# Performance work log

Hardware: AMD Instinct MI355X
Metric: run time of the kernel (lower is better)

Reference implementation:

```python
import jax, jax.numpy as jnp
import numpy as np

B, T, C, H = 2, 2048, 1024, 16
HID = 4096
EPS = 1e-5
NEG_INF = float('-inf')


def layer_norm(x, w, b):
    mu = jnp.mean(x, axis=-1, keepdims=True)
    var = jnp.mean((x - mu) ** 2, axis=-1, keepdims=True)
    return (x - mu) / jnp.sqrt(var + EPS) * w + b


def setup_inputs() -> dict:
    key = jax.random.key(0)
    ks = jax.random.split(key, 12)
    s = lambda fan_in: 1.0 / np.sqrt(fan_in)
    return {
        'x': jax.random.normal(ks[0], (B, T, C), dtype=jnp.float32),
        'mask': jax.random.randint(ks[1], (B, T), 0, 2) > 0,
        'attn_w': jax.random.normal(ks[2], (C, 3 * C), dtype=jnp.float32) * s(C),
        'attn_b': jnp.zeros((3 * C,), dtype=jnp.float32),
        'proj_w': jax.random.normal(ks[3], (C, C), dtype=jnp.float32) * s(C),
        'proj_b': jnp.zeros((C,), dtype=jnp.float32),
        'ln1_w': jnp.ones((C,), dtype=jnp.float32),
        'ln1_b': jnp.zeros((C,), dtype=jnp.float32),
        'lin1_w': jax.random.normal(ks[4], (C, HID), dtype=jnp.float32) * s(C),
        'lin1_b': jnp.zeros((HID,), dtype=jnp.float32),
        'lin2_w': jax.random.normal(ks[5], (HID, C), dtype=jnp.float32) * s(HID),
        'lin2_b': jnp.zeros((C,), dtype=jnp.float32),
        'ln2_w': jnp.ones((C,), dtype=jnp.float32),
        'ln2_b': jnp.zeros((C,), dtype=jnp.float32),
    }


def reference(x, mask, attn_w, attn_b, proj_w, proj_b, ln1_w, ln1_b,
              lin1_w, lin1_b, lin2_w, lin2_b, ln2_w, ln2_b):
    D = C // H
    # fused QKV projection
    qkv = x @ attn_w + attn_b                      # [B,T,3C]
    q, k, v = jnp.split(qkv, 3, axis=-1)
    q = q.reshape(B, T, H, D).transpose(0, 2, 1, 3)  # [B,H,T,D]
    k = k.reshape(B, T, H, D).transpose(0, 2, 1, 3)
    v = v.reshape(B, T, H, D).transpose(0, 2, 1, 3)
    scale = 1.0 / jnp.sqrt(jnp.asarray(D, dtype=q.dtype))
    scores = jnp.einsum('bhqd,bhkd->bhqk', q, k) * scale  # [B,H,T,T]
    # bidirectional padding mask with forced-true first key column
    m2d = mask[:, None, :] & mask[:, :, None]       # [B,T,T]
    m2d = m2d.at[:, :, 0].set(True)
    bias = jnp.where(m2d, 0.0, NEG_INF).astype(scores.dtype)
    scores = scores + bias[:, None, :, :]
    w = jax.nn.softmax(scores, axis=-1)
    w = jnp.nan_to_num(w, nan=0.0, posinf=0.0, neginf=0.0)
    y = jnp.einsum('bhqk,bhkd->bhqd', w, v)
    y = y.transpose(0, 2, 1, 3).reshape(B, T, C)
    y = y @ proj_w + proj_b
    # residual + post-LN, then MLP + residual + post-LN
    h = layer_norm(x + y, ln1_w, ln1_b)
    ff = jax.nn.gelu(h @ lin1_w + lin1_b, approximate=False) @ lin2_w + lin2_b
    return layer_norm(h + ff, ln2_w, ln2_b)
```

## Files before the change

### kernel.cpp

```cpp
#include <hip/hip_runtime.h>
#include <hip/hip_bf16.h>
#include <math.h>

typedef __attribute__((ext_vector_type(4))) float f32x4;
typedef __attribute__((ext_vector_type(8))) __bf16 bf16x8v;
typedef __attribute__((ext_vector_type(4))) __bf16 bf16x4v;
typedef __attribute__((ext_vector_type(4))) short s16x4;
typedef __attribute__((ext_vector_type(4))) unsigned short u16x4;

#define AS1(p) ((const __attribute__((address_space(1))) void*)(p))
#define AS3(p) ((__attribute__((address_space(3))) void*)(p))

__device__ __forceinline__ unsigned short f2bf(float f) {
  union { __bf16 b; unsigned short u; } cv;
  cv.b = (__bf16)f;
  return cv.u;
}

__device__ __forceinline__ f32x4 mfma32(bf16x8v a, bf16x8v b, f32x4 c) {
  return __builtin_amdgcn_mfma_f32_16x16x32_bf16(a, b, c, 0, 0, 0);
}

__device__ __forceinline__ f32x4 mfma16(s16x4 a, s16x4 b, f32x4 c) {
#if __has_builtin(__builtin_amdgcn_mfma_f32_16x16x16bf16_1k)
  return __builtin_amdgcn_mfma_f32_16x16x16bf16_1k(a, b, c, 0, 0, 0);
#elif __has_builtin(__builtin_amdgcn_mfma_f32_16x16x16_bf16)
  bf16x4v av, bv;
  __builtin_memcpy(&av, &a, 8);
  __builtin_memcpy(&bv, &b, 8);
  return __builtin_amdgcn_mfma_f32_16x16x16_bf16(av, bv, c, 0, 0, 0);
#else
  asm volatile("v_mfma_f32_16x16x16_bf16 %0, %1, %2, %0\n\ts_nop 7\n\ts_nop 7\n\ts_nop 7"
               : "+v"(c) : "v"(a), "v"(b));
  return c;
#endif
}

__device__ __forceinline__ void async_copy16(const void* g, void* l) {
  __builtin_amdgcn_global_load_lds(AS1(g), AS3(l), 16, 0, 0);
}

__global__ __launch_bounds__(256) void cvt_bf16_kernel(const float* __restrict__ in,
                                                       unsigned short* __restrict__ out, int n4) {
  int i = blockIdx.x * 256 + threadIdx.x;
  if (i < n4) {
    f32x4 v = ((const f32x4*)in)[i];
    u16x4 o;
    o.x = f2bf(v.x); o.y = f2bf(v.y); o.z = f2bf(v.z); o.w = f2bf(v.w);
    ((u16x4*)out)[i] = o;
  }
}

__global__ __launch_bounds__(256) void wtrans_kernel(const float* __restrict__ W,
                                                     unsigned short* __restrict__ Wt,
                                                     int Kd, int Nd) {
  __shared__ float t[32][33];
  int tx = threadIdx.x & 31, ty = threadIdx.x >> 5;
  int bx = blockIdx.x, by = blockIdx.y;
  for (int i = 0; i < 4; ++i) {
    int r = by * 32 + ty + i * 8, c = bx * 32 + tx;
    t[ty + i * 8][tx] = W[(size_t)r * Nd + c];
  }
  __syncthreads();
  for (int i = 0; i < 4; ++i) {
    int nn = bx * 32 + ty + i * 8, kk = by * 32 + tx;
    Wt[(size_t)nn * Kd + kk] = f2bf(t[tx][ty + i * 8]);
  }
}

template <int EPI>
__global__ __launch_bounds__(512, 2) void gemm256(const unsigned short* __restrict__ A,
                                                  const unsigned short* __restrict__ Bt,
                                                  const float* __restrict__ bias,
                                                  unsigned short* __restrict__ out,
                                                  int M, int N, int Kd, int gx) {
  __shared__ __align__(16) unsigned short Al[2][256 * 64];
  __shared__ __align__(16) unsigned short Bl[2][256 * 64];
  int tid = threadIdx.x, wid = tid >> 6, lane = tid & 63;
  int lo = lane & 15, hi = lane >> 4;
  int wm = wid >> 2, wn = wid & 3;

  int wg = blockIdx.x, nwg = gridDim.x;
  int cpx = nwg >> 3;
  int swz = (wg & 7) * cpx + (wg >> 3);
  int m0 = (swz / gx) * 256, n0 = (swz % gx) * 256;

  f32x4 acc[8][4];
#pragma unroll
  for (int mf = 0; mf < 8; ++mf)
#pragma unroll
    for (int nf = 0; nf < 4; ++nf) acc[mf][nf] = f32x4{0.f, 0.f, 0.f, 0.f};

  int nkt = Kd >> 6;

  auto stageAB = [&](int buf, int kt) {
#pragma unroll
    for (int i = 0; i < 4; ++i) {
      int G = (wid * 4 + i) * 64 + lane;
      int row = G >> 3, c16 = G & 7;
      int csw = ((c16 ^ (row & 7)) << 3);
      const unsigned short* ga = A + ((size_t)(m0 + row)) * Kd + kt * 64 + csw;
      async_copy16(ga, &Al[buf][(wid * 4 + i) * 512]);
      const unsigned short* gb = Bt + ((size_t)(n0 + row)) * Kd + kt * 64 + csw;
      async_copy16(gb, &Bl[buf][(wid * 4 + i) * 512]);
    }
  };

  stageAB(0, 0);
  int cur = 0;
  for (int t = 0; t < nkt; ++t) {
    __builtin_amdgcn_s_barrier();
    int nx = t + 1 < nkt ? t + 1 : nkt - 1;
    stageAB(cur ^ 1, nx);
    asm volatile("s_waitcnt vmcnt(8)" ::: "memory");
    __builtin_amdgcn_sched_barrier(0);

    bf16x8v bfr[4][2];
#pragma unroll
    for (int nf = 0; nf < 4; ++nf) {
      int rb = wn * 64 + nf * 16 + lo;
#pragma unroll
      for (int kh = 0; kh < 2; ++kh)
        bfr[nf][kh] = *(const bf16x8v*)&Bl[cur][rb * 64 + (((kh * 4 + hi) ^ (rb & 7)) << 3)];
    }
#pragma unroll
    for (int q = 0; q < 4; ++q) {
      bf16x8v afr[2][2];
#pragma unroll
      for (int m2 = 0; m2 < 2; ++m2) {
        int ra = wm * 128 + (q * 2 + m2) * 16 + lo;
#pragma unroll
        for (int kh = 0; kh < 2; ++kh)
          afr[m2][kh] = *(const bf16x8v*)&Al[cur][ra * 64 + (((kh * 4 + hi) ^ (ra & 7)) << 3)];
      }
      __builtin_amdgcn_s_setprio(1);
#pragma unroll
      for (int m2 = 0; m2 < 2; ++m2)
#pragma unroll
        for (int nf = 0; nf < 4; ++nf) {
          acc[q * 2 + m2][nf] = mfma32(afr[m2][0], bfr[nf][0], acc[q * 2 + m2][nf]);
          acc[q * 2 + m2][nf] = mfma32(afr[m2][1], bfr[nf][1], acc[q * 2 + m2][nf]);
        }
      __builtin_amdgcn_s_setprio(0);
    }
    cur ^= 1;
  }

#pragma unroll
  for (int nf = 0; nf < 4; ++nf) {
    int col = n0 + wn * 64 + nf * 16 + lo;
    float bv = bias[col];
#pragma unroll
    for (int mf = 0; mf < 8; ++mf) {
      int row0 = m0 + wm * 128 + mf * 16 + hi * 4;
#pragma unroll
      for (int j = 0; j < 4; ++j) {
        float v = acc[mf][nf][j] + bv;
        if (EPI == 2) v = 0.5f * v * (1.f + erff(v * 0.70710678118654752f));
        out[(size_t)(row0 + j) * N + col] = f2bf(v);
      }
    }
  }
}

template <int EPI>
__global__ __launch_bounds__(256) void gemm_bt(const unsigned short* __restrict__ A,
                                               const unsigned short* __restrict__ Bt,
                                               const float* __restrict__ bias,
                                               void* __restrict__ out,
                                               int M, int N, int Kd, int gx) {
  __shared__ __align__(16) unsigned short As[3][128 * 32];
  __shared__ __align__(16) unsigned short Bs[3][128 * 32];
  int tid = threadIdx.x, wid = tid >> 6, lane = tid & 63;
  int lo = lane & 15, hi = lane >> 4;

  int wg = blockIdx.x, nwg = gridDim.x;
  int cpx = nwg >> 3;
  int swz = (wg & 7) * cpx + (wg >> 3);
  int m0 = (swz / gx) * 128, n0 = (swz % gx) * 128;

  int wm = wid >> 1, wn = wid & 1;
  f32x4 acc[4][4];
  for (int m = 0; m < 4; ++m)
    for (int n = 0; n < 4; ++n) acc[m][n] = f32x4{0.f, 0.f, 0.f, 0.f};
  int sr = lane >> 2;
  int sc = (lane & 3) * 8;
  int nkt = Kd >> 5;

  auto stage = [&](int buf, int kt) {
    int k0 = kt * 32;
#pragma unroll
    for (int i = 0; i < 2; ++i) {
      int ch = wid * 2 + i;
      const unsigned short* ga = A + ((size_t)(m0 + ch * 16 + sr)) * Kd + k0 + sc;
      async_copy16(ga, &As[buf][ch * 512]);
      const unsigned short* gb = Bt + ((size_t)(n0 + ch * 16 + sr)) * Kd + k0 + sc;
      async_copy16(gb, &Bs[buf][ch * 512]);
    }
  };

  stage(0, 0);
  stage(1, 1);
  stage(2, 2);
  int cur = 0;
  for (int kt = 0; kt < nkt; ++kt) {
    asm volatile("s_waitcnt vmcnt(8)" ::: "memory");
    asm volatile("s_barrier" ::: "memory");
    __builtin_amdgcn_sched_barrier(0);
    bf16x8v af[4], bf_[4];
#pragma unroll
    for (int m = 0; m < 4; ++m)
      af[m] = *(const bf16x8v*)&As[cur][(wm * 64 + m * 16 + lo) * 32 + hi * 8];
#pragma unroll
    for (int n = 0; n < 4; ++n)
      bf_[n] = *(const bf16x8v*)&Bs[cur][(wn * 64 + n * 16 + lo) * 32 + hi * 8];
#pragma unroll
    for (int m = 0; m < 4; ++m)
#pragma unroll
      for (int n = 0; n < 4; ++n)
        acc[m][n] = mfma32(af[m], bf_[n], acc[m][n]);
    __builtin_amdgcn_sched_barrier(0);
    asm volatile("s_barrier" ::: "memory");
    int nx = kt + 3;
    nx = nx < nkt ? nx : nkt - 1;
    stage(cur, nx);
    cur = cur + 1;
    cur = cur == 3 ? 0 : cur;
  }

#pragma unroll
  for (int n = 0; n < 4; ++n) {
    int col = n0 + wn * 64 + n * 16 + lo;
    float bv = bias ? bias[col] : 0.f;
#pragma unroll
    for (int m = 0; m < 4; ++m) {
      int row0 = m0 + wm * 64 + m * 16 + hi * 4;
#pragma unroll
      for (int j = 0; j < 4; ++j) {
        float v = acc[m][n][j] + bv;
        size_t idx = (size_t)(row0 + j) * N + col;
        if (EPI == 1) ((float*)out)[idx] = v;
        else          ((unsigned short*)out)[idx] = f2bf(v);
      }
    }
  }
}

__global__ __launch_bounds__(256) void reshape_qk_kernel(const unsigned short* __restrict__ qkv,
                                                         unsigned short* __restrict__ Q,
                                                         unsigned short* __restrict__ K) {
  int idx = blockIdx.x * 256 + threadIdx.x;
  int row = idx >> 9;
  int g = idx & 511;
  int col = g * 4;
  int sec = col >> 10;
  int cc = col & 1023;
  int h = cc >> 6, d = cc & 63;
  int b = row >> 11, t = row & 2047;
  u16x4 v = *(const u16x4*)&qkv[(size_t)row * 3072 + col];
  unsigned short* dst = sec ? K : Q;
  *(u16x4*)&dst[(((size_t)(b * 16 + h)) * 2048 + t) * 64 + d] = v;
}

__global__ __launch_bounds__(256) void vtrans_kernel(const unsigned short* __restrict__ qkv,
                                                     unsigned short* __restrict__ Vt) {
  __shared__ unsigned short t[32][33];
  int tx = threadIdx.x & 31, ty = threadIdx.x >> 5;
  int bx = blockIdx.x, dt = blockIdx.y, bh = blockIdx.z;
  int b = bh >> 4, h = bh & 15;
  for (int i = 0; i < 4; ++i) {
    int trow = bx * 32 + ty + i * 8;
    t[ty + i * 8][tx] = qkv[((size_t)(b * 2048 + trow)) * 3072 + 2048 + h * 64 + dt * 32 + tx];
  }
  __syncthreads();
  for (int i = 0; i < 4; ++i) {
    int d = dt * 32 + ty + i * 8;
    int trow = bx * 32 + tx;
    Vt[((size_t)bh * 64 + d) * 2048 + trow] = t[tx][ty + i * 8];
  }
}

__global__ __launch_bounds__(256) void attn_kernel(const unsigned short* __restrict__ Q,
                                                   const unsigned short* __restrict__ Kt,
                                                   const unsigned short* __restrict__ Vt,
                                                   const int* __restrict__ mask,
                                                   unsigned short* __restrict__ Y) {
  __shared__ __align__(16) unsigned short Kl[2][4096];
  __shared__ __align__(16) unsigned short Vl[2][4096];
  __shared__ float sbias[2048];

  int qt = blockIdx.x, bh = blockIdx.y;
  int b = bh >> 4, h = bh & 15;
  int tid = threadIdx.x, wv = tid >> 6, lane = tid & 63;
  int lo = lane & 15, hi = lane >> 4;

  for (int k = tid; k < 2048; k += 256) {
    int mk = mask[b * 2048 + k];
    sbias[k] = (mk != 0 || k == 0) ? 0.f : -1e30f;
  }

  int r8 = lane >> 3;
  int jsrc = (((lane & 7) ^ r8) << 4);
  const size_t kvbase = (size_t)bh * 2048;

  auto stage = [&](int buf, int kt2) {
    int kbase = kt2 * 64;
#pragma unroll
    for (int i = 0; i < 2; ++i) {
      int r = i * 32 + wv * 8 + r8;
      const unsigned short* gk = Kt + (kvbase + kbase + r) * 64 + (jsrc >> 1);
      async_copy16(gk, (char*)Kl + buf * 8192 + i * 4096 + wv * 1024);
      const unsigned short* gv = Vt + ((size_t)bh * 64 + r) * 2048 + kbase + (jsrc >> 1);
      async_copy16(gv, (char*)Vl + buf * 8192 + i * 4096 + wv * 1024);
    }
  };

  int qrow = qt * 64 + wv * 16 + lo;
  size_t qoff = (kvbase + qrow) * 64;
  bf16x8v Qf0 = *(const bf16x8v*)(Q + qoff + hi * 8);
  bf16x8v Qf1 = *(const bf16x8v*)(Q + qoff + 32 + hi * 8);
  float qm = (mask[b * 2048 + qrow] != 0) ? -16.f : -1e30f;

  const float scale2 = 0.125f * 1.44269504088896340736f;
  float l_run = 0.f;
  f32x4 acc[4];
#pragma unroll
  for (int c = 0; c < 4; ++c) acc[c] = f32x4{0.f, 0.f, 0.f, 0.f};

  stage(0, 0);
  stage(1, 1);
  asm volatile("s_waitcnt lgkmcnt(0)" ::: "memory");

  int sw = (lo & 7) << 4;
  int cur = 0;
  for (int kt = 0; kt < 32; ++kt) {
    asm volatile("s_waitcnt vmcnt(4)" ::: "memory");
    asm volatile("s_barrier" ::: "memory");
    __builtin_amdgcn_sched_barrier(0);
    int kbase = kt * 64;

    f32x4 s4[4];
#pragma unroll
    for (int kb = 0; kb < 4; ++kb) {
      const char* kr = (const char*)Kl + cur * 8192 + (kb * 16 + lo) * 128;
      bf16x8v K0 = *(const bf16x8v*)(kr + ((hi * 16) ^ sw));
      bf16x8v K1 = *(const bf16x8v*)(kr + ((64 + hi * 16) ^ sw));
      f32x4 z = f32x4{0.f, 0.f, 0.f, 0.f};
      z = mfma32(K0, Qf0, z);
      z = mfma32(K1, Qf1, z);
      s4[kb] = z;
    }

    float p[16];
#pragma unroll
    for (int kb = 0; kb < 4; ++kb) {
      f32x4 bb = *(const f32x4*)&sbias[kbase + kb * 16 + hi * 4];
#pragma unroll
      for (int r = 0; r < 4; ++r)
        p[kb * 4 + r] = fmaf(s4[kb][r], scale2, bb[r] + qm);
    }
    if (kt == 0)
      p[0] = (hi == 0) ? fmaf(s4[0][0], scale2, -16.f) : p[0];
#pragma unroll
    for (int i = 0; i < 16; ++i) p[i] = exp2f(p[i]);
    float ls0 = 0.f, ls1 = 0.f;
#pragma unroll
    for (int i = 0; i < 8; ++i) { ls0 += p[i]; ls1 += p[8 + i]; }
    l_run += ls0 + ls1;

    union { __bf16 b[4]; s16x4 s4v; } pk[4];
#pragma unroll
    for (int kb = 0; kb < 4; ++kb)
#pragma unroll
      for (int r = 0; r < 4; ++r) pk[kb].b[r] = (__bf16)p[kb * 4 + r];

#pragma unroll
    for (int c = 0; c < 4; ++c) {
      const char* vr = (const char*)Vl + cur * 8192 + (c * 16 + lo) * 128;
#pragma unroll
      for (int kk = 0; kk < 4; ++kk) {
        s16x4 V0 = *(const s16x4*)(vr + ((kk * 32 + hi * 8) ^ sw));
        acc[c] = mfma16(V0, pk[kk].s4v, acc[c]);
      }
    }
    __builtin_amdgcn_sched_barrier(0);
    asm volatile("s_barrier" ::: "memory");
    int nx = kt + 2;
    nx = nx < 32 ? nx : 31;
    stage(cur, nx);
    cur ^= 1;
  }

  l_run += __shfl_xor(l_run, 16);
  l_run += __shfl_xor(l_run, 32);
  float invl = 1.f / l_run;
  size_t yrow = ((size_t)(b * 2048 + qrow)) * 1024 + h * 64;
#pragma unroll
  for (int c = 0; c < 4; ++c)
#pragma unroll
    for (int r = 0; r < 4; ++r)
      Y[yrow + c * 16 + hi * 4 + r] = f2bf(acc[c][r] * invl);
}

__global__ __launch_bounds__(256) void ln_kernel(const float* __restrict__ A,
                                                 const float* __restrict__ Bsrc,
                                                 const float* __restrict__ w,
                                                 const float* __restrict__ bias,
                                                 float* __restrict__ outF,
                                                 unsigned short* __restrict__ outB) {
  int row = blockIdx.x, tid = threadIdx.x;
  f32x4 r = ((const f32x4*)A)[row * 256 + tid] + ((const f32x4*)Bsrc)[row * 256 + tid];
  float s = r.x + r.y + r.z + r.w;
  float q = r.x * r.x + r.y * r.y + r.z * r.z + r.w * r.w;
  for (int off = 1; off < 64; off <<= 1) {
    s += __shfl_xor(s, off);
    q += __shfl_xor(q, off);
  }
  __shared__ float ls[4], lq[4];
  int wid = tid >> 6, lane = tid & 63;
  if (lane == 0) { ls[wid] = s; lq[wid] = q; }
  __syncthreads();
  s = ls[0] + ls[1] + ls[2] + ls[3];
  q = lq[0] + lq[1] + lq[2] + lq[3];
  float mu = s * (1.f / 1024.f);
  float var = q * (1.f / 1024.f) - mu * mu;
  float rstd = rsqrtf(var + 1e-5f);
  f32x4 wv = ((const f32x4*)w)[tid];
  f32x4 bv = ((const f32x4*)bias)[tid];
  f32x4 o = (r - mu) * rstd * wv + bv;
  if (outF) ((f32x4*)outF)[row * 256 + tid] = o;
  if (outB) {
    u16x4 ob;
    ob.x = f2bf(o.x); ob.y = f2bf(o.y); ob.z = f2bf(o.z); ob.w = f2bf(o.w);
    ((u16x4*)outB)[row * 256 + tid] = ob;
  }
}

extern "C" void kernel_launch(void* const* d_in, const int* in_sizes, int n_in,
                              void* d_out, int out_size, void* d_ws, size_t ws_size,
                              hipStream_t stream) {
  const float* x      = (const float*)d_in[0];
  const int*   mask   = (const int*)d_in[1];
  const float* attn_w = (const float*)d_in[2];
  const float* attn_b = (const float*)d_in[3];
  const float* proj_w = (const float*)d_in[4];
  const float* proj_b = (const float*)d_in[5];
  const float* ln1_w  = (const float*)d_in[6];
  const float* ln1_b  = (const float*)d_in[7];
  const float* lin1_w = (const float*)d_in[8];
  const float* lin1_b = (const float*)d_in[9];
  const float* lin2_w = (const float*)d_in[10];
  const float* lin2_b = (const float*)d_in[11];
  const float* ln2_w  = (const float*)d_in[12];
  const float* ln2_b  = (const float*)d_in[13];
  float* out = (float*)d_out;

  char* ws = (char*)d_ws;
  size_t off = 0;
  auto alloc = [&](size_t bytes) { char* p = ws + off; off += (bytes + 255) & ~(size_t)255; return p; };

  unsigned short* attn_wT = (unsigned short*)alloc((size_t)3072 * 1024 * 2);
  unsigned short* proj_wT = (unsigned short*)alloc((size_t)1024 * 1024 * 2);
  unsigned short* lin1_wT = (unsigned short*)alloc((size_t)4096 * 1024 * 2);
  unsigned short* lin2_wT = (unsigned short*)alloc((size_t)1024 * 4096 * 2);
  char* regionA = alloc((size_t)3 * 8388608);
  char* regionB = alloc((size_t)8388608);
  char* regionC = alloc((size_t)25165824);
  float* h_f32  = (float*)alloc((size_t)4096 * 1024 * 4);
  unsigned short* h_bf16 = (unsigned short*)alloc((size_t)4096 * 1024 * 2);
  float* mlp2   = (float*)alloc((size_t)4096 * 1024 * 4);

  unsigned short* Qb  = (unsigned short*)regionA;
  unsigned short* Kb  = (unsigned short*)(regionA + 8388608);
  unsigned short* Vtb = (unsigned short*)(regionA + 16777216);
  unsigned short* ff1 = (unsigned short*)regionA;
  unsigned short* xb  = (unsigned short*)regionB;
  unsigned short* qkv = (unsigned short*)regionC;
  unsigned short* Yb  = (unsigned short*)regionC;
  float* proj_out     = (float*)(regionC + 8388608);

  wtrans_kernel<<<dim3(96, 32), 256, 0, stream>>>(attn_w, attn_wT, 1024, 3072);
  wtrans_kernel<<<dim3(32, 32), 256, 0, stream>>>(proj_w, proj_wT, 1024, 1024);
  wtrans_kernel<<<dim3(128, 32), 256, 0, stream>>>(lin1_w, lin1_wT, 1024, 4096);
  wtrans_kernel<<<dim3(32, 128), 256, 0, stream>>>(lin2_w, lin2_wT, 4096, 1024);
  cvt_bf16_kernel<<<4096, 256, 0, stream>>>(x, xb, 4096 * 1024 / 4);

  gemm256<0><<<192, 512, 0, stream>>>(xb, attn_wT, attn_b, qkv, 4096, 3072, 1024, 12);
  reshape_qk_kernel<<<8192, 256, 0, stream>>>(qkv, Qb, Kb);
  vtrans_kernel<<<dim3(64, 2, 32), 256, 0, stream>>>(qkv, Vtb);

  attn_kernel<<<dim3(32, 32), 256, 0, stream>>>(Qb, Kb, Vtb, mask, Yb);

  gemm_bt<1><<<256, 256, 0, stream>>>(Yb, proj_wT, proj_b, proj_out, 4096, 1024, 1024, 8);
  ln_kernel<<<4096, 256, 0, stream>>>(x, proj_out, ln1_w, ln1_b, h_f32, h_bf16);

  gemm256<2><<<256, 512, 0, stream>>>(h_bf16, lin1_wT, lin1_b, ff1, 4096, 4096, 1024, 16);
  gemm_bt<1><<<256, 256, 0, stream>>>(ff1, lin2_wT, lin2_b, mlp2, 4096, 1024, 4096, 8);
  ln_kernel<<<4096, 256, 0, stream>>>(h_f32, mlp2, ln2_w, ln2_b, out, nullptr);
}
```

Baseline: 440.7 us.

## Read Q/K directly from qkv, split-K lin2 GEMM, widen attention blocks

The Q/K reshape kernel is removed, and attention now loads Q and K straight from the packed qkv buffer using 512-thread blocks that each cover 128 query rows. The lin2 GEMM is split along K into two halves that write separate fp32 partials, doubling the grid to 512 workgroups, and the second layernorm sums both partials. Scheduling barriers and setprio hints are also dropped from the GEMM and attention loops. The changes target a launch plus a memory pass and low occupancy in lin2, at the cost of an extra fp32 partial buffer and strided K loads.

```diff
diff --git a/kernel.cpp b/kernel.cpp
--- a/kernel.cpp
+++ b/kernel.cpp
@@ -113,7 +113,6 @@
     int nx = t + 1 < nkt ? t + 1 : nkt - 1;
     stageAB(cur ^ 1, nx);
     asm volatile("s_waitcnt vmcnt(8)" ::: "memory");
-    __builtin_amdgcn_sched_barrier(0);
 
     bf16x8v bfr[4][2];
 #pragma unroll
@@ -133,7 +132,6 @@
         for (int kh = 0; kh < 2; ++kh)
           afr[m2][kh] = *(const bf16x8v*)&Al[cur][ra * 64 + (((kh * 4 + hi) ^ (ra & 7)) << 3)];
       }
-      __builtin_amdgcn_s_setprio(1);
 #pragma unroll
       for (int m2 = 0; m2 < 2; ++m2)
 #pragma unroll
@@ -141,7 +139,6 @@
           acc[q * 2 + m2][nf] = mfma32(afr[m2][0], bfr[nf][0], acc[q * 2 + m2][nf]);
           acc[q * 2 + m2][nf] = mfma32(afr[m2][1], bfr[nf][1], acc[q * 2 + m2][nf]);
         }
-      __builtin_amdgcn_s_setprio(0);
     }
     cur ^= 1;
   }
@@ -163,21 +160,29 @@
   }
 }
 
-template <int EPI>
+template <int EPI, int SPLIT>
 __global__ __launch_bounds__(256) void gemm_bt(const unsigned short* __restrict__ A,
                                                const unsigned short* __restrict__ Bt,
                                                const float* __restrict__ bias,
-                                               void* __restrict__ out,
-                                               int M, int N, int Kd, int gx) {
+                                               void* __restrict__ out0,
+                                               void* __restrict__ out1,
+                                               int M, int N, int Kd, int ldk, int gx) {
   __shared__ __align__(16) unsigned short As[3][128 * 32];
   __shared__ __align__(16) unsigned short Bs[3][128 * 32];
   int tid = threadIdx.x, wid = tid >> 6, lane = tid & 63;
   int lo = lane & 15, hi = lane >> 4;
 
   int wg = blockIdx.x, nwg = gridDim.x;
+  int kp = 0;
+  if (SPLIT) { kp = wg & 1; wg >>= 1; nwg >>= 1; }
   int cpx = nwg >> 3;
   int swz = (wg & 7) * cpx + (wg >> 3);
   int m0 = (swz / gx) * 128, n0 = (swz % gx) * 128;
+
+  const unsigned short* Ab = A + (SPLIT ? kp * Kd : 0);
+  const unsigned short* Bb = Bt + (SPLIT ? kp * Kd : 0);
+  void* out = (SPLIT && kp) ? out1 : out0;
+  const float* bz = (SPLIT && kp) ? nullptr : bias;
 
   int wm = wid >> 1, wn = wid & 1;
   f32x4 acc[4][4];
@@ -192,9 +197,9 @@
 #pragma unroll
     for (int i = 0; i < 2; ++i) {
       int ch = wid * 2 + i;
-      const unsigned short* ga = A + ((size_t)(m0 + ch * 16 + sr)) * Kd + k0 + sc;
+      const unsigned short* ga = Ab + ((size_t)(m0 + ch * 16 + sr)) * ldk + k0 + sc;
       async_copy16(ga, &As[buf][ch * 512]);
-      const unsigned short* gb = Bt + ((size_t)(n0 + ch * 16 + sr)) * Kd + k0 + sc;
+      const unsigned short* gb = Bb + ((size_t)(n0 + ch * 16 + sr)) * ldk + k0 + sc;
       async_copy16(gb, &Bs[buf][ch * 512]);
     }
   };
@@ -206,7 +211,6 @@
   for (int kt = 0; kt < nkt; ++kt) {
     asm volatile("s_waitcnt vmcnt(8)" ::: "memory");
     asm volatile("s_barrier" ::: "memory");
-    __builtin_amdgcn_sched_barrier(0);
     bf16x8v af[4], bf_[4];
 #pragma unroll
     for (int m = 0; m < 4; ++m)
@@ -219,7 +223,6 @@
 #pragma unroll
       for (int n = 0; n < 4; ++n)
         acc[m][n] = mfma32(af[m], bf_[n], acc[m][n]);
-    __builtin_amdgcn_sched_barrier(0);
     asm volatile("s_barrier" ::: "memory");
     int nx = kt + 3;
     nx = nx < nkt ? nx : nkt - 1;
@@ -231,7 +234,7 @@
 #pragma unroll
   for (int n = 0; n < 4; ++n) {
     int col = n0 + wn * 64 + n * 16 + lo;
-    float bv = bias ? bias[col] : 0.f;
+    float bv = bz ? bz[col] : 0.f;
 #pragma unroll
     for (int m = 0; m < 4; ++m) {
       int row0 = m0 + wm * 64 + m * 16 + hi * 4;
@@ -244,22 +247,6 @@
       }
     }
   }
-}
-
-__global__ __launch_bounds__(256) void reshape_qk_kernel(const unsigned short* __restrict__ qkv,
-                                                         unsigned short* __restrict__ Q,
-                                                         unsigned short* __restrict__ K) {
-  int idx = blockIdx.x * 256 + threadIdx.x;
-  int row = idx >> 9;
-  int g = idx & 511;
-  int col = g * 4;
-  int sec = col >> 10;
-  int cc = col & 1023;
-  int h = cc >> 6, d = cc & 63;
-  int b = row >> 11, t = row & 2047;
-  u16x4 v = *(const u16x4*)&qkv[(size_t)row * 3072 + col];
-  unsigned short* dst = sec ? K : Q;
-  *(u16x4*)&dst[(((size_t)(b * 16 + h)) * 2048 + t) * 64 + d] = v;
 }
 
 __global__ __launch_bounds__(256) void vtrans_kernel(const unsigned short* __restrict__ qkv,
@@ -280,8 +267,7 @@
   }
 }
 
-__global__ __launch_bounds__(256) void attn_kernel(const unsigned short* __restrict__ Q,
-                                                   const unsigned short* __restrict__ Kt,
+__global__ __launch_bounds__(512) void attn_kernel(const unsigned short* __restrict__ qkv,
                                                    const unsigned short* __restrict__ Vt,
                                                    const int* __restrict__ mask,
                                                    unsigned short* __restrict__ Y) {
@@ -294,31 +280,28 @@
   int tid = threadIdx.x, wv = tid >> 6, lane = tid & 63;
   int lo = lane & 15, hi = lane >> 4;
 
-  for (int k = tid; k < 2048; k += 256) {
+  for (int k = tid; k < 2048; k += 512) {
     int mk = mask[b * 2048 + k];
     sbias[k] = (mk != 0 || k == 0) ? 0.f : -1e30f;
   }
 
-  int r8 = lane >> 3;
-  int jsrc = (((lane & 7) ^ r8) << 4);
-  const size_t kvbase = (size_t)bh * 2048;
+  int r = tid >> 3;
+  int slot = tid & 7;
+  int jb = ((slot ^ (r & 7)) << 4) >> 1;
 
   auto stage = [&](int buf, int kt2) {
     int kbase = kt2 * 64;
-#pragma unroll
-    for (int i = 0; i < 2; ++i) {
-      int r = i * 32 + wv * 8 + r8;
-      const unsigned short* gk = Kt + (kvbase + kbase + r) * 64 + (jsrc >> 1);
-      async_copy16(gk, (char*)Kl + buf * 8192 + i * 4096 + wv * 1024);
-      const unsigned short* gv = Vt + ((size_t)bh * 64 + r) * 2048 + kbase + (jsrc >> 1);
-      async_copy16(gv, (char*)Vl + buf * 8192 + i * 4096 + wv * 1024);
-    }
+    const unsigned short* gk =
+        qkv + ((size_t)(b * 2048 + kbase + r)) * 3072 + 1024 + h * 64 + jb;
+    async_copy16(gk, (char*)Kl + buf * 8192 + wv * 1024);
+    const unsigned short* gv = Vt + ((size_t)(bh * 64 + r)) * 2048 + kbase + jb;
+    async_copy16(gv, (char*)Vl + buf * 8192 + wv * 1024);
   };
 
-  int qrow = qt * 64 + wv * 16 + lo;
-  size_t qoff = (kvbase + qrow) * 64;
-  bf16x8v Qf0 = *(const bf16x8v*)(Q + qoff + hi * 8);
-  bf16x8v Qf1 = *(const bf16x8v*)(Q + qoff + 32 + hi * 8);
+  int qrow = qt * 128 + wv * 16 + lo;
+  const unsigned short* qp = qkv + ((size_t)(b * 2048 + qrow)) * 3072 + h * 64;
+  bf16x8v Qf0 = *(const bf16x8v*)(qp + hi * 8);
+  bf16x8v Qf1 = *(const bf16x8v*)(qp + 32 + hi * 8);
   float qm = (mask[b * 2048 + qrow] != 0) ? -16.f : -1e30f;
 
   const float scale2 = 0.125f * 1.44269504088896340736f;
@@ -334,9 +317,8 @@
   int sw = (lo & 7) << 4;
   int cur = 0;
   for (int kt = 0; kt < 32; ++kt) {
-    asm volatile("s_waitcnt vmcnt(4)" ::: "memory");
+    asm volatile("s_waitcnt vmcnt(2)" ::: "memory");
     asm volatile("s_barrier" ::: "memory");
-    __builtin_amdgcn_sched_barrier(0);
     int kbase = kt * 64;
 
     f32x4 s4[4];
@@ -356,8 +338,8 @@
     for (int kb = 0; kb < 4; ++kb) {
       f32x4 bb = *(const f32x4*)&sbias[kbase + kb * 16 + hi * 4];
 #pragma unroll
-      for (int r = 0; r < 4; ++r)
-        p[kb * 4 + r] = fmaf(s4[kb][r], scale2, bb[r] + qm);
+      for (int rr = 0; rr < 4; ++rr)
+        p[kb * 4 + rr] = fmaf(s4[kb][rr], scale2, bb[rr] + qm);
     }
     if (kt == 0)
       p[0] = (hi == 0) ? fmaf(s4[0][0], scale2, -16.f) : p[0];
@@ -372,7 +354,7 @@
 #pragma unroll
     for (int kb = 0; kb < 4; ++kb)
 #pragma unroll
-      for (int r = 0; r < 4; ++r) pk[kb].b[r] = (__bf16)p[kb * 4 + r];
+      for (int rr = 0; rr < 4; ++rr) pk[kb].b[rr] = (__bf16)p[kb * 4 + rr];
 
 #pragma unroll
     for (int c = 0; c < 4; ++c) {
@@ -383,7 +365,6 @@
         acc[c] = mfma16(V0, pk[kk].s4v, acc[c]);
       }
     }
-    __builtin_amdgcn_sched_barrier(0);
     asm volatile("s_barrier" ::: "memory");
     int nx = kt + 2;
     nx = nx < 32 ? nx : 31;
@@ -398,18 +379,20 @@
 #pragma unroll
   for (int c = 0; c < 4; ++c)
 #pragma unroll
-    for (int r = 0; r < 4; ++r)
-      Y[yrow + c * 16 + hi * 4 + r] = f2bf(acc[c][r] * invl);
+    for (int rr = 0; rr < 4; ++rr)
+      Y[yrow + c * 16 + hi * 4 + rr] = f2bf(acc[c][rr] * invl);
 }
 
 __global__ __launch_bounds__(256) void ln_kernel(const float* __restrict__ A,
-                                                 const float* __restrict__ Bsrc,
+                                                 const float* __restrict__ B1,
+                                                 const float* __restrict__ B2,
                                                  const float* __restrict__ w,
                                                  const float* __restrict__ bias,
                                                  float* __restrict__ outF,
                                                  unsigned short* __restrict__ outB) {
   int row = blockIdx.x, tid = threadIdx.x;
-  f32x4 r = ((const f32x4*)A)[row * 256 + tid] + ((const f32x4*)Bsrc)[row * 256 + tid];
+  f32x4 r = ((const f32x4*)A)[row * 256 + tid] + ((const f32x4*)B1)[row * 256 + tid];
+  if (B2) r += ((const f32x4*)B2)[row * 256 + tid];
   float s = r.x + r.y + r.z + r.w;
   float q = r.x * r.x + r.y * r.y + r.z * r.z + r.w * r.w;
   for (int off = 1; off < 64; off <<= 1) {
@@ -463,21 +446,17 @@
   unsigned short* proj_wT = (unsigned short*)alloc((size_t)1024 * 1024 * 2);
   unsigned short* lin1_wT = (unsigned short*)alloc((size_t)4096 * 1024 * 2);
   unsigned short* lin2_wT = (unsigned short*)alloc((size_t)1024 * 4096 * 2);
-  char* regionA = alloc((size_t)3 * 8388608);
-  char* regionB = alloc((size_t)8388608);
-  char* regionC = alloc((size_t)25165824);
-  float* h_f32  = (float*)alloc((size_t)4096 * 1024 * 4);
+  unsigned short* qkv     = (unsigned short*)alloc((size_t)4096 * 3072 * 2);
+  unsigned short* Vtb     = (unsigned short*)alloc((size_t)32 * 64 * 2048 * 2);
+  unsigned short* xb      = (unsigned short*)alloc((size_t)4096 * 1024 * 2);
+  float* proj_out = (float*)alloc((size_t)4096 * 1024 * 4);
+  float* h_f32    = (float*)alloc((size_t)4096 * 1024 * 4);
   unsigned short* h_bf16 = (unsigned short*)alloc((size_t)4096 * 1024 * 2);
-  float* mlp2   = (float*)alloc((size_t)4096 * 1024 * 4);
-
-  unsigned short* Qb  = (unsigned short*)regionA;
-  unsigned short* Kb  = (unsigned short*)(regionA + 8388608);
-  unsigned short* Vtb = (unsigned short*)(regionA + 16777216);
-  unsigned short* ff1 = (unsigned short*)regionA;
-  unsigned short* xb  = (unsigned short*)regionB;
-  unsigned short* qkv = (unsigned short*)regionC;
-  unsigned short* Yb  = (unsigned short*)regionC;
-  float* proj_out     = (float*)(regionC + 8388608);
+  float* mlp2a   = (float*)alloc((size_t)4096 * 1024 * 4);
+  float* mlp2b   = (float*)alloc((size_t)4096 * 1024 * 4);
+
+  unsigned short* ff1 = qkv;
+  unsigned short* Yb  = xb;
 
   wtrans_kernel<<<dim3(96, 32), 256, 0, stream>>>(attn_w, attn_wT, 1024, 3072);
   wtrans_kernel<<<dim3(32, 32), 256, 0, stream>>>(proj_w, proj_wT, 1024, 1024);
@@ -486,15 +465,16 @@
   cvt_bf16_kernel<<<4096, 256, 0, stream>>>(x, xb, 4096 * 1024 / 4);
 
   gemm256<0><<<192, 512, 0, stream>>>(xb, attn_wT, attn_b, qkv, 4096, 3072, 1024, 12);
-  reshape_qk_kernel<<<8192, 256, 0, stream>>>(qkv, Qb, Kb);
   vtrans_kernel<<<dim3(64, 2, 32), 256, 0, stream>>>(qkv, Vtb);
 
-  attn_kernel<<<dim3(32, 32), 256, 0, stream>>>(Qb, Kb, Vtb, mask, Yb);
-
-  gemm_bt<1><<<256, 256, 0, stream>>>(Yb, proj_wT, proj_b, proj_out, 4096, 1024, 1024, 8);
-  ln_kernel<<<4096, 256, 0, stream>>>(x, proj_out, ln1_w, ln1_b, h_f32, h_bf16);
+  attn_kernel<<<dim3(16, 32), 512, 0, stream>>>(qkv, Vtb, mask, Yb);
+
+  gemm_bt<1, 0><<<256, 256, 0, stream>>>(Yb, proj_wT, proj_b, proj_out, nullptr,
+                                         4096, 1024, 1024, 1024, 8);
+  ln_kernel<<<4096, 256, 0, stream>>>(x, proj_out, nullptr, ln1_w, ln1_b, h_f32, h_bf16);
 
   gemm256<2><<<256, 512, 0, stream>>>(h_bf16, lin1_wT, lin1_b, ff1, 4096, 4096, 1024, 16);
-  gemm_bt<1><<<256, 256, 0, stream>>>(ff1, lin2_wT, lin2_b, mlp2, 4096, 1024, 4096, 8);
-  ln_kernel<<<4096, 256, 0, stream>>>(h_f32, mlp2, ln2_w, ln2_b, out, nullptr);
-}
+  gemm_bt<1, 1><<<512, 256, 0, stream>>>(ff1, lin2_wT, lin2_b, mlp2a, mlp2b,
+                                         4096, 1024, 2048, 4096, 8);
+  ln_kernel<<<4096, 256, 0, stream>>>(h_f32, mlp2a, mlp2b, ln2_w, ln2_b, out, nullptr);
+}
```

Result: faster. 399.5 us (-9.3%).
